# Kernel optimization log

Hardware: AMD Instinct MI355X
Metric: run time of the kernel (lower is better)

## Reference

```python
import jax, jax.numpy as jnp
import numpy as np

C = 10  # cluster gap window; repo-level global constant in the original code


def _per_neuron(v, label):
    """Faithful vectorized translation of the per-(batch,neuron) Python loops.

    v:     [T] membrane potential trace
    label: scalar int target cluster count
    Returns (loss_contribution, num_cluster).
    """
    T = v.shape[0]
    t = jnp.arange(T, dtype=jnp.int32)
    spk = v >= 0.0                                   # spike positions (v >= 0)
    # exclusive prefix counts of spikes: csp[i] = #spikes in v[:i]
    csp = jnp.concatenate([jnp.zeros(1, jnp.int32), jnp.cumsum(spk.astype(jnp.int32))])
    lo = jnp.clip(t - C, 0, T)
    # a spike starts a new cluster iff no spike in the preceding C steps
    cnt_prev = csp[t] - csp[lo]
    is_start = spk & (cnt_prev == 0)
    num_cluster = jnp.sum(is_start.astype(jnp.int32))
    vmax = jnp.max(v)

    # ---- excess branch (label > num_cluster) ----
    # mask[t] = 1 iff some spike lies in [t-C, t+C]  (union of [first-C, last+C] per cluster)
    hi = jnp.clip(t + C + 1, 0, T)
    mask = (csp[hi] - csp[lo]) > 0
    full0 = jnp.all(mask)
    NEG = jnp.asarray(-1e30, v.dtype)
    m0 = jnp.max(jnp.where(mask, NEG, v))            # max over unmasked times (iter 0)
    tm = jnp.argmax(v)                               # original uses global argmax of v
    win = (t >= tm - C // 2) & (t <= tm + C // 2)
    mask2 = mask | win                               # mask after first loop iteration (fixed thereafter)
    full2 = jnp.all(mask2)
    # if mask2 full, remaining iterations pick a spike value (random in original; spikes have v>=0,
    # we use the deterministic surrogate vmax which is always a spike value when spikes exist)
    m_rest = jnp.where(full2, vmax, jnp.max(jnp.where(mask2, NEG, v)))
    label_f = label.astype(v.dtype)
    ncf = num_cluster.astype(v.dtype)
    dE = jnp.maximum(label_f - ncf, 1.0)             # safe denominator (branch-gated below)
    mean_excess = (m0 + (dE - 1.0) * m_rest) / dE
    excess_loss = jnp.where(full0, vmax, -mean_excess)

    # ---- deficit branch (label < num_cluster) ----
    BIG = T + 2 * C + 2
    lt = jax.lax.cummax(jnp.where(spk, t, -BIG))                 # nearest spike <= t
    rt = jax.lax.cummin(jnp.where(spk, t, BIG)[::-1])[::-1]      # nearest spike >= t
    in_span = (rt - lt) <= C                                     # t inside [first,last] of a cluster
    cid = jnp.cumsum(is_start.astype(jnp.int32)) - 1             # cluster id at time t
    K = T // (C + 1) + 1                                         # max possible clusters
    seg = jnp.where(in_span, cid, K)
    rec = jax.ops.segment_max(v, seg, num_segments=K + 1)[:K]    # per-cluster span max
    POS = jnp.asarray(1e30, v.dtype)
    rec = jnp.where(jnp.arange(K) < num_cluster, rec, POS)
    rec = jnp.sort(rec)                                          # ascending, real clusters first
    dD = jnp.maximum(ncf - label_f, 1.0)
    deficit_loss = jnp.sum(jnp.where(jnp.arange(K) < (num_cluster - label), rec, 0.0)) / dD

    contrib = jnp.where(label > num_cluster, excess_loss,
                        jnp.where(label < num_cluster, deficit_loss, 0.0))
    return contrib, num_cluster


def setup_inputs() -> dict:
    key = jax.random.key(0)
    k1, k2, k3 = jax.random.split(key, 3)
    B, T, N = 256, 500, 128
    vmem = jax.random.normal(k1, (B, T, N), dtype=jnp.float32)
    vlastmem = jax.random.normal(k2, (B, T, N), dtype=jnp.float32)
    labels_t = jax.random.randint(k3, (B, N), 0, 5, dtype=jnp.int32)
    return {"vmem": vmem, "vlastmem": vlastmem, "labels_t": labels_t, "ratio": 1}


def reference(vmem, vlastmem, labels_t, ratio):
    # vlastmem and ratio are unused in the original forward; kept for signature fidelity.
    vv = jnp.transpose(vmem, (0, 2, 1))  # [B, N, T]
    contrib, nclus = jax.vmap(jax.vmap(_per_neuron))(vv, labels_t)
    loss = jnp.sum(contrib)
    spike_output = nclus.astype(jnp.float32)  # [B, N] cluster counts
    return loss, spike_output
```

## Files before the change

kernel.cpp:

```cpp
#include <hip/hip_runtime.h>

namespace {
constexpr int CC   = 10;
constexpr int TT   = 500;
constexpr int NN   = 128;
constexpr int G    = 10;
constexpr int LSEG = TT / G;
constexpr int HALO = CC;
constexpr int NB   = 32;
constexpr int MAXG = TT / (CC + 1) + 1;
}

__global__ __launch_bounds__(320, 5)
void fused_kernel(const float* __restrict__ vmem, const int* __restrict__ labels,
                  float* __restrict__ out) {
    const int tid = threadIdx.x;
    const int g   = tid >> 5;
    const int ln  = tid & 31;
    const int b   = blockIdx.y;
    const int n   = (blockIdx.x << 5) | ln;
    const int a   = g * LSEG;
    const bool firstSeg = (g == 0), lastSeg = (g == G - 1);
    const float* __restrict__ col = vmem + (size_t)b * TT * NN + n;

    __shared__ float s_rec[G][10][NB];
    __shared__ float s_gl[MAXG][NB];
    __shared__ float wb[512];

    float b0[10], b1[10], b2[10], b3[10] = {};

    auto load = [&](float (&d)[10], int c) {
        if ((firstSeg && c == 0) || (lastSeg && c == 6)) {
            #pragma unroll
            for (int j = 0; j < 10; ++j) {
                int t = a + (-HALO + 10 * c + j);
                t = t < 0 ? 0 : (t > TT - 1 ? TT - 1 : t);
                d[j] = col[t * NN];
            }
        } else {
            const float* __restrict__ p = col + (a - HALO + 10 * c) * NN;
            #pragma unroll
            for (int j = 0; j < 10; ++j) d[j] = p[j * NN];
        }
    };

    int   ls = -(1 << 20), lcount = 0, hdne = 0, tmn = 0, hasu = 0;
    float ccm = -1e30f, rmax = -1e30f, hdm = -1e30f, vmx = -1e30f, m0 = -1e30f;

    auto scan = [&](const float (&cur)[10], const float (&prev)[10], int c) {
        #pragma unroll
        for (int j = 0; j < 10; ++j) {
            const int ofs = -HALO + 10 * c + j;
            const int t   = a + ofs;
            float v = cur[j];
            if ((ofs < 0 && firstSeg) || (ofs >= LSEG && lastSeg)) v = -1.0f;
            const bool spike = v >= 0.0f;
            if (ofs >= 0 && ofs < LSEG) {
                const float rm2 = fmaxf(rmax, v);
                if (spike) {
                    if (t - ls > CC) {
                        if (lcount > 0) s_rec[g][lcount - 1][ln] = ccm;
                        ccm = v; ++lcount;
                    } else if (lcount == 0) { hdne = 1; hdm = fmaxf(hdm, rm2); }
                    else ccm = fmaxf(ccm, rm2);
                    rmax = -1e30f;
                } else rmax = rm2;
                if (v > vmx) { vmx = v; tmn = t; }
            }
            if (spike) ls = t;
            if (ofs >= HALO) {
                const float vu = prev[j];
                if (ls < t - 2 * CC) { hasu = 1; if (vu > m0) m0 = vu; }
            }
        }
    };

    #define SB __builtin_amdgcn_sched_barrier(0)
    load(b0, 0); load(b1, 1); SB;
    load(b2, 2); SB; scan(b0, b3, 0); SB;
    load(b3, 3); SB; scan(b1, b0, 1); SB;
    load(b0, 4); SB; scan(b2, b1, 2); SB;
    load(b1, 5); SB; scan(b3, b2, 3); SB;
    load(b2, 6); SB; scan(b0, b3, 4); SB;
    scan(b1, b0, 5); scan(b2, b1, 6);
    #undef SB

    if (lcount > 0) s_rec[g][lcount - 1][ln] = ccm;

    s_rec[g][5][ln] = __int_as_float(lcount | (hdne << 3) | (hasu << 4) | (tmn << 5));
    s_rec[g][6][ln] = hdm;
    s_rec[g][7][ln] = rmax;
    s_rec[g][8][ln] = vmx;
    s_rec[g][9][ln] = m0;
    __syncthreads();

    if (tid < NB) {
        int gi = 0, g_nc = 0, g_hasu = 0, g_tm = 0;
        bool open = false; float cur = -1e30f, ptg = -1e30f;
        float g_vmax = -1e30f, g_m0 = -1e30f;
        #pragma unroll
        for (int s2 = 0; s2 < G; ++s2) {
            const int pk = __float_as_int(s_rec[s2][5][tid]);
            const int k = pk & 7, hne = (pk >> 3) & 1;
            g_nc += k; g_hasu |= (pk >> 4) & 1;
            const float vmS = s_rec[s2][8][tid];
            if (vmS > g_vmax) { g_vmax = vmS; g_tm = pk >> 5; }
            const float m0S = s_rec[s2][9][tid];
            if (m0S > g_m0) g_m0 = m0S;
            if (open) {
                if (hne) { cur = fmaxf(cur, fmaxf(ptg, s_rec[s2][6][tid]));
                           ptg = s_rec[s2][7][tid]; }
                if (k > 0 || !hne) { s_gl[gi][tid] = cur; ++gi; open = false; }
            }
            if (k > 0) {
                for (int i = 0; i < k - 1; ++i) { s_gl[gi][tid] = s_rec[s2][i][tid]; ++gi; }
                cur = s_rec[s2][k - 1][tid]; open = true; ptg = s_rec[s2][7][tid];
            }
        }
        if (open) { s_gl[gi][tid] = cur; ++gi; }

        const int label = labels[b * NN + n];

        const bool need2 = (label > g_nc) && g_hasu && (label - g_nc >= 2);
        float mrest = g_vmax;
        unsigned long long bal = __ballot(need2);
        const float* colbase = vmem + (size_t)b * TT * NN;
        while (bal) {
            const int fl = __ffsll(bal) - 1;
            bal &= bal - 1;
            const int   nf    = (blockIdx.x << 5) | fl;
            const int   tmf   = __shfl(g_tm, fl);
            const float vmaxf = __shfl(g_vmax, fl);
            #pragma unroll
            for (int j = 0; j < 16; ++j) {
                const int t = tid * 16 + j;
                wb[t] = (t < TT) ? colbase[(size_t)t * NN + nf] : -1.0f;
            }
            asm volatile("s_waitcnt lgkmcnt(0)" ::: "memory");
            __builtin_amdgcn_wave_barrier();
            int ls2 = -1000, lh = 0; float lm = -1e30f;
            const int u0 = tid * 16;
            for (int t2 = u0 - 10; t2 < u0 + 26; ++t2) {
                const float v = (t2 >= 0 && t2 < 512) ? wb[t2] : -1.0f;
                if (v >= 0.0f) ls2 = t2;
                const int u = t2 - 10;
                if (u >= u0 && u < u0 + 16 && u < TT) {
                    if (ls2 < u - 10 && (u < tmf - CC / 2 || u > tmf + CC / 2)) {
                        lh = 1; const float vu = wb[u]; if (vu > lm) lm = vu;
                    }
                }
            }
            #pragma unroll
            for (int off = 16; off > 0; off >>= 1) {
                lm = fmaxf(lm, __shfl_down(lm, off));
                lh |= __shfl_down(lh, off);
            }
            const float res = __shfl(lh ? lm : vmaxf, 0);
            if (tid == fl) mrest = res;
            __builtin_amdgcn_wave_barrier();
        }

        float contrib = 0.0f;
        if (label > g_nc) {
            if (!g_hasu) contrib = g_vmax;
            else {
                const float dE = (float)(label - g_nc);
                contrib = -((g_m0 + (dE - 1.0f) * mrest) / dE);
            }
        } else if (label < g_nc) {
            const int kk = g_nc - label;
            float ssum = 0.0f;
            for (int i = 0; i < kk; ++i) {
                float mn = 1e30f; int mj = 0;
                for (int jj = 0; jj < g_nc; ++jj) {
                    const float x = s_gl[jj][tid];
                    if (x < mn) { mn = x; mj = jj; }
                }
                ssum += mn; s_gl[mj][tid] = 1e30f;
            }
            contrib = ssum / (float)kk;
        }

        out[1 + b * NN + n] = (float)g_nc;

        float w = contrib;
        #pragma unroll
        for (int off = 16; off > 0; off >>= 1) w += __shfl_down(w, off);
        if (tid == 0) atomicAdd(out, w);
    }
}

extern "C" void kernel_launch(void* const* d_in, const int* in_sizes, int n_in,
                              void* d_out, int out_size, void* d_ws, size_t ws_size,
                              hipStream_t stream) {
    const float* vmem   = (const float*)d_in[0];
    const int*   labels = (const int*)d_in[2];
    float*       out    = (float*)d_out;
    (void)d_ws; (void)ws_size;

    const int B = in_sizes[2] / NN;

    hipMemsetAsync(out, 0, sizeof(float), stream);
    hipLaunchKernelGGL(fused_kernel, dim3(NN / NB, B), dim3(G * NB), 0, stream,
                       vmem, labels, out);
}
```

Before: 167.3 us.

## Load whole segment into registers up front instead of rotating software pipeline

Replaces the four rotating 10-element register buffers and the interleaved load/scan schedule with a single 70-element register array. All loads are issued at once before a single unrolled scan. Occupancy hint is lowered from 5 to 4 blocks per SM to make room for the extra registers. This gives the memory system more loads in flight per thread, at the cost of higher register pressure and fewer resident waves.

```diff
diff --git a/kernel.cpp b/kernel.cpp
--- a/kernel.cpp
+++ b/kernel.cpp
@@ -1,17 +1,18 @@
 #include <hip/hip_runtime.h>
 
 namespace {
-constexpr int CC   = 10;
-constexpr int TT   = 500;
-constexpr int NN   = 128;
-constexpr int G    = 10;
-constexpr int LSEG = TT / G;
-constexpr int HALO = CC;
-constexpr int NB   = 32;
-constexpr int MAXG = TT / (CC + 1) + 1;
+constexpr int CC    = 10;
+constexpr int TT    = 500;
+constexpr int NN    = 128;
+constexpr int G     = 10;
+constexpr int LSEG  = TT / G;
+constexpr int HALO  = CC;
+constexpr int NB    = 32;
+constexpr int NELEM = LSEG + 2 * HALO;
+constexpr int MAXG  = TT / (CC + 1) + 1;
 }
 
-__global__ __launch_bounds__(320, 5)
+__global__ __launch_bounds__(320, 4)
 void fused_kernel(const float* __restrict__ vmem, const int* __restrict__ labels,
                   float* __restrict__ out) {
     const int tid = threadIdx.x;
@@ -27,64 +28,44 @@
     __shared__ float s_gl[MAXG][NB];
     __shared__ float wb[512];
 
-    float b0[10], b1[10], b2[10], b3[10] = {};
-
-    auto load = [&](float (&d)[10], int c) {
-        if ((firstSeg && c == 0) || (lastSeg && c == 6)) {
-            #pragma unroll
-            for (int j = 0; j < 10; ++j) {
-                int t = a + (-HALO + 10 * c + j);
-                t = t < 0 ? 0 : (t > TT - 1 ? TT - 1 : t);
-                d[j] = col[t * NN];
-            }
-        } else {
-            const float* __restrict__ p = col + (a - HALO + 10 * c) * NN;
-            #pragma unroll
-            for (int j = 0; j < 10; ++j) d[j] = p[j * NN];
-        }
-    };
+    float r[NELEM];
+    #pragma unroll
+    for (int i = 0; i < NELEM; ++i) {
+        int t = a + i - HALO;
+        if (i < HALO)          t = t < 0 ? 0 : t;
+        if (i >= LSEG + HALO)  t = t > TT - 1 ? TT - 1 : t;
+        r[i] = col[t * NN];
+    }
+    __builtin_amdgcn_sched_barrier(0);
 
     int   ls = -(1 << 20), lcount = 0, hdne = 0, tmn = 0, hasu = 0;
     float ccm = -1e30f, rmax = -1e30f, hdm = -1e30f, vmx = -1e30f, m0 = -1e30f;
 
-    auto scan = [&](const float (&cur)[10], const float (&prev)[10], int c) {
-        #pragma unroll
-        for (int j = 0; j < 10; ++j) {
-            const int ofs = -HALO + 10 * c + j;
-            const int t   = a + ofs;
-            float v = cur[j];
-            if ((ofs < 0 && firstSeg) || (ofs >= LSEG && lastSeg)) v = -1.0f;
-            const bool spike = v >= 0.0f;
-            if (ofs >= 0 && ofs < LSEG) {
-                const float rm2 = fmaxf(rmax, v);
-                if (spike) {
-                    if (t - ls > CC) {
-                        if (lcount > 0) s_rec[g][lcount - 1][ln] = ccm;
-                        ccm = v; ++lcount;
-                    } else if (lcount == 0) { hdne = 1; hdm = fmaxf(hdm, rm2); }
-                    else ccm = fmaxf(ccm, rm2);
-                    rmax = -1e30f;
-                } else rmax = rm2;
-                if (v > vmx) { vmx = v; tmn = t; }
-            }
-            if (spike) ls = t;
-            if (ofs >= HALO) {
-                const float vu = prev[j];
-                if (ls < t - 2 * CC) { hasu = 1; if (vu > m0) m0 = vu; }
-            }
+    #pragma unroll
+    for (int i = 0; i < NELEM; ++i) {
+        const int ofs = i - HALO;
+        const int t   = a + ofs;
+        float v = r[i];
+        if ((ofs < 0 && firstSeg) || (ofs >= LSEG && lastSeg)) v = -1.0f;
+        const bool spike = v >= 0.0f;
+        if (ofs >= 0 && ofs < LSEG) {
+            const float rm2 = fmaxf(rmax, v);
+            if (spike) {
+                if (t - ls > CC) {
+                    if (lcount > 0) s_rec[g][lcount - 1][ln] = ccm;
+                    ccm = v; ++lcount;
+                } else if (lcount == 0) { hdne = 1; hdm = fmaxf(hdm, rm2); }
+                else ccm = fmaxf(ccm, rm2);
+                rmax = -1e30f;
+            } else rmax = rm2;
+            if (v > vmx) { vmx = v; tmn = t; }
         }
-    };
-
-    #define SB __builtin_amdgcn_sched_barrier(0)
-    load(b0, 0); load(b1, 1); SB;
-    load(b2, 2); SB; scan(b0, b3, 0); SB;
-    load(b3, 3); SB; scan(b1, b0, 1); SB;
-    load(b0, 4); SB; scan(b2, b1, 2); SB;
-    load(b1, 5); SB; scan(b3, b2, 3); SB;
-    load(b2, 6); SB; scan(b0, b3, 4); SB;
-    scan(b1, b0, 5); scan(b2, b1, 6);
-    #undef SB
-
+        if (spike) ls = t;
+        if (ofs >= HALO) {
+            const float vu = r[i - 10];
+            if (ls < t - 2 * CC) { hasu = 1; if (vu > m0) m0 = vu; }
+        }
+    }
     if (lcount > 0) s_rec[g][lcount - 1][ln] = ccm;
 
     s_rec[g][5][ln] = __int_as_float(lcount | (hdne << 3) | (hasu << 4) | (tmn << 5));
```

Result: slower. 181.8 us (+8.7%).
